# Performance work log

Hardware: AMD Instinct MI355X
Metric: run time of the kernel (lower is better)

Reference implementation:

```python
import jax, jax.numpy as jnp
import numpy as np

B, T, D, L, H = 16, 2048, 512, 6, 1024  # batch, seq, embed_dim, num_layers, mlp hidden (2*D)
K = D // 2  # freq bands; k = min(D//2, T//2) = 256 here
VOCAB = 256


def _ln(x, g, b, eps=1e-5):
    m = x.mean(-1, keepdims=True)
    v = ((x - m) ** 2).mean(-1, keepdims=True)
    return (x - m) / jnp.sqrt(v + eps) * g + b


def setup_inputs() -> dict:
    key = jax.random.key(0)
    ks = jax.random.split(key, 12)
    s = 0.02
    return {
        "byte_ids": jax.random.randint(ks[0], (B, T), 0, 256),
        # ByteSpectralEmbedding params
        "freq_bands": jnp.ones((K,), jnp.float32),
        "fp_w1": jax.random.normal(ks[1], (D, 2 * D), jnp.float32) * s,
        "fp_b1": jnp.zeros((2 * D,), jnp.float32),
        "fp_ln_g": jnp.ones((2 * D,), jnp.float32),
        "fp_ln_b": jnp.zeros((2 * D,), jnp.float32),
        "fp_w2": jax.random.normal(ks[2], (2 * D, D), jnp.float32) * s,
        "fp_b2": jnp.zeros((D,), jnp.float32),
        # SpectralMLPBlock params, stacked over L layers (FNet-style spectral mixing + MLP)
        "blk_ln1_g": jnp.ones((L, D), jnp.float32),
        "blk_ln1_b": jnp.zeros((L, D), jnp.float32),
        "blk_ln2_g": jnp.ones((L, D), jnp.float32),
        "blk_ln2_b": jnp.zeros((L, D), jnp.float32),
        "blk_w1": jax.random.normal(ks[3], (L, D, H), jnp.float32) * s,
        "blk_b1": jnp.zeros((L, H), jnp.float32),
        "blk_w2": jax.random.normal(ks[4], (L, H, D), jnp.float32) * s,
        "blk_b2": jnp.zeros((L, D), jnp.float32),
        # final norm + output head
        "norm_g": jnp.ones((D,), jnp.float32),
        "norm_b": jnp.zeros((D,), jnp.float32),
        "out_w": jax.random.normal(ks[5], (D, VOCAB), jnp.float32) * s,
        "out_b": jnp.zeros((VOCAB,), jnp.float32),
    }


def reference(byte_ids, freq_bands, fp_w1, fp_b1, fp_ln_g, fp_ln_b, fp_w2, fp_b2,
              blk_ln1_g, blk_ln1_b, blk_ln2_g, blk_ln2_b, blk_w1, blk_b1, blk_w2, blk_b2,
              norm_g, norm_b, out_w, out_b):
    Bc, Tc = byte_ids.shape
    k = min(D // 2, Tc // 2)
    signal = byte_ids.astype(jnp.float32) / 127.5 - 1.0          # [B,T]
    X = jnp.fft.fft(signal, axis=1)[:, :k]                        # [B,k] single FFT
    # shift theorem: FFT(roll(signal, -p))[f] = X[f] * exp(+2pi i f p / T)
    mag = jnp.abs(X) * freq_bands[:k]                             # [B,k], position-independent
    base_phase = jnp.angle(X)                                     # [B,k]
    pos = jnp.arange(Tc, dtype=jnp.float32)
    f = jnp.arange(k, dtype=jnp.float32)
    phase = base_phase[:, None, :] + (2.0 * jnp.pi / Tc) * pos[None, :, None] * f[None, None, :]  # [B,T,k]
    mag_bt = jnp.broadcast_to(mag[:, None, :], (Bc, Tc, k))
    feats = jnp.concatenate([mag_bt, jnp.sin(phase), jnp.cos(phase)], axis=-1)
    feats = feats[..., :D] if feats.shape[-1] >= D else jnp.pad(feats, ((0, 0), (0, 0), (0, D - feats.shape[-1])))
    # freq_proj: Linear -> LayerNorm -> GELU -> Linear
    h = feats @ fp_w1 + fp_b1
    h = jax.nn.gelu(_ln(h, fp_ln_g, fp_ln_b), approximate=False)
    x = h @ fp_w2 + fp_b2                                         # [B,T,D]
    # SpectralMLPBlock stack: residual FFT mixing + residual MLP
    for i in range(L):
        y = _ln(x, blk_ln1_g[i], blk_ln1_b[i])
        x = x + jnp.fft.fft(jnp.fft.fft(y, axis=-1), axis=1).real
        y = _ln(x, blk_ln2_g[i], blk_ln2_b[i])
        x = x + jax.nn.gelu(y @ blk_w1[i] + blk_b1[i], approximate=False) @ blk_w2[i] + blk_b2[i]
    x = _ln(x, norm_g, norm_b)
    return x @ out_w + out_b                                      # [B,T,256]
```

## Files before the change

kernel.cpp:

```cpp
#include <hip/hip_runtime.h>
#include <cmath>

typedef unsigned short u16;
typedef unsigned int u32;

constexpr int NB = 16;
constexpr int NT = 2048;
constexpr int ND = 512;
constexpr int NL = 6;
constexpr int NH = 1024;
constexpr int NK = 256;
constexpr int NM = NB * NT;

constexpr float PI2 = 6.283185307179586f;

typedef short bf16x8 __attribute__((ext_vector_type(8)));
typedef float f32x4 __attribute__((ext_vector_type(4)));

__device__ __forceinline__ float gelu_exact(float v) {
    return 0.5f * v * (1.0f + erff(v * 0.70710678118654752f));
}

__device__ __forceinline__ u16 f2bf(float f) {
    union { float f; u32 u; } v; v.f = f;
    u32 r = v.u + 0x7FFFu + ((v.u >> 16) & 1u);
    return (u16)(r >> 16);
}

__device__ __forceinline__ float bf2f(u16 h) {
    union { u32 u; float f; } v; v.u = ((u32)h) << 16;
    return v.f;
}

__device__ __forceinline__ float block_sum256(float val, float* lds4) {
#pragma unroll
    for (int o = 32; o > 0; o >>= 1) val += __shfl_down(val, o);
    int lane = threadIdx.x & 63, wid = threadIdx.x >> 6;
    if (lane == 0) lds4[wid] = val;
    __syncthreads();
    float t = lds4[0] + lds4[1] + lds4[2] + lds4[3];
    __syncthreads();
    return t;
}

__device__ __forceinline__ void swz_block(int& row0, int& col0) {
    int nwg = gridDim.x * gridDim.y;
    int wg = blockIdx.x + blockIdx.y * gridDim.x;
    int L = wg;
    if ((nwg & 7) == 0) {
        int q = nwg >> 3;
        L = (wg & 7) * q + (wg >> 3);
    }
    int ncol = gridDim.y;
    row0 = (L / ncol) * 128;
    col0 = (L % ncol) * 128;
}

__global__ void twiddle_kernel(float2* __restrict__ tw) {
    int idx = blockIdx.x * 256 + threadIdx.x;
    if (idx < 2047) {
        u32 v = idx + 1;
        u32 h = 1u << (31 - __clz(v));
        u32 k = v - h;
        float a = -(float)M_PI * (float)k / (float)h;
        tw[idx] = make_float2(cosf(a), sinf(a));
    }
}

__global__ void dft_kernel(const int* __restrict__ bytes, const float* __restrict__ fb,
                           float* __restrict__ mag, float* __restrict__ cph,
                           float* __restrict__ sph) {
    __shared__ float lr[4], li[4];
    int b = blockIdx.x, f = blockIdx.y;
    float re = 0.f, im = 0.f;
    for (int t = threadIdx.x; t < NT; t += 256) {
        float s = (float)bytes[b * NT + t] * (1.0f / 127.5f) - 1.0f;
        int idx = (t * f) & (NT - 1);
        float a = (float)idx * (PI2 / NT);
        float sn, cs;
        sincosf(a, &sn, &cs);
        re += s * cs;
        im -= s * sn;
    }
#pragma unroll
    for (int o = 32; o > 0; o >>= 1) {
        re += __shfl_down(re, o);
        im += __shfl_down(im, o);
    }
    int lane = threadIdx.x & 63, wid = threadIdx.x >> 6;
    if (lane == 0) { lr[wid] = re; li[wid] = im; }
    __syncthreads();
    if (threadIdx.x == 0) {
        float R = lr[0] + lr[1] + lr[2] + lr[3];
        float I = li[0] + li[1] + li[2] + li[3];
        float m = sqrtf(R * R + I * I);
        mag[b * NK + f] = m * fb[f];
        float inv = (m > 0.f) ? 1.0f / m : 0.f;
        cph[b * NK + f] = (m > 0.f) ? R * inv : 1.0f;
        sph[b * NK + f] = I * inv;
    }
}

__global__ void feats_split_kernel(const float* __restrict__ mag,
                                   const float* __restrict__ cph,
                                   const float* __restrict__ sph,
                                   u16* __restrict__ hi, u16* __restrict__ lo) {
    int idx = blockIdx.x * 256 + threadIdx.x;
    int d = idx & (ND - 1);
    int m = idx >> 9;
    int b = m >> 11, t = m & (NT - 1);
    float v;
    if (d < NK) {
        v = mag[b * NK + d];
    } else {
        int f = d - NK;
        int a = (t * f) & (NT - 1);
        float sn, cs;
        sincosf((float)a * (PI2 / NT), &sn, &cs);
        v = sph[b * NK + f] * cs + cph[b * NK + f] * sn;
    }
    u16 h = f2bf(v);
    hi[idx] = h;
    lo[idx] = f2bf(v - bf2f(h));
}

template <int NV, int GELU, int OBF>
__global__ void ln_kernel(const float* __restrict__ in, const float* __restrict__ g,
                          const float* __restrict__ bta, void* __restrict__ outv) {
    __shared__ float lds4[4];
    constexpr int NE = NV / 256;
    size_t row = blockIdx.x;
    const float* p = in + row * NV;
    float v[NE];
    float sum = 0.f;
#pragma unroll
    for (int i = 0; i < NE; ++i) {
        v[i] = p[threadIdx.x + 256 * i];
        sum += v[i];
    }
    sum = block_sum256(sum, lds4);
    float mean = sum * (1.0f / NV);
    float sq = 0.f;
#pragma unroll
    for (int i = 0; i < NE; ++i) {
        float d = v[i] - mean;
        sq += d * d;
    }
    sq = block_sum256(sq, lds4);
    float inv = rsqrtf(sq * (1.0f / NV) + 1e-5f);
#pragma unroll
    for (int i = 0; i < NE; ++i) {
        int c = threadIdx.x + 256 * i;
        float r = (v[i] - mean) * inv * g[c] + bta[c];
        if (GELU) r = gelu_exact(r);
        if (OBF == 2) {
            u16* o = (u16*)outv + row * (2 * NV);
            u16 hb = f2bf(r);
            o[c] = hb;
            o[NV + c] = f2bf(r - bf2f(hb));
        } else if (OBF == 1) {
            ((u16*)outv)[row * NV + c] = f2bf(r);
        } else {
            ((float*)outv)[row * NV + c] = r;
        }
    }
}

__global__ void ln_fftd_kernel(const float* __restrict__ x, const float* __restrict__ g,
                               const float* __restrict__ bta, float* __restrict__ P,
                               const float2* __restrict__ twid) {
    __shared__ float sr[2][512], si[2][512];
    __shared__ float red[2][2];
    int sub = threadIdx.x >> 7;
    int tid = threadIdx.x & 127;
    int rlocal = blockIdx.x * 2 + sub;
    const float* p = x + (size_t)rlocal * ND;
    float v[4];
    float s = 0.f;
#pragma unroll
    for (int j = 0; j < 4; ++j) { v[j] = p[tid + 128 * j]; s += v[j]; }
#pragma unroll
    for (int o = 32; o > 0; o >>= 1) s += __shfl_down(s, o);
    int wv = (threadIdx.x >> 6) & 1;
    if ((threadIdx.x & 63) == 0) red[sub][wv] = s;
    __syncthreads();
    float mean = (red[sub][0] + red[sub][1]) * (1.0f / ND);
    float q = 0.f;
#pragma unroll
    for (int j = 0; j < 4; ++j) { float d = v[j] - mean; q += d * d; }
#pragma unroll
    for (int o = 32; o > 0; o >>= 1) q += __shfl_down(q, o);
    __syncthreads();
    if ((threadIdx.x & 63) == 0) red[sub][wv] = q;
    __syncthreads();
    float inv = rsqrtf((red[sub][0] + red[sub][1]) * (1.0f / ND) + 1e-5f);
#pragma unroll
    for (int j = 0; j < 4; ++j) {
        int i = tid + 128 * j;
        int r = __brev((unsigned)i) >> 23;
        sr[sub][r] = (v[j] - mean) * inv * g[i] + bta[i];
        si[sub][r] = 0.f;
    }
    __syncthreads();
    for (int len = 2; len <= 512; len <<= 1) {
        int half = len >> 1;
        for (int qq = tid; qq < 256; qq += 128) {
            int k = qq & (half - 1);
            int j = ((qq - k) << 1) + k;
            float2 tw = twid[(half - 1) + k];
            float cs = tw.x, sn = tw.y;
            float ur = sr[sub][j], ui = si[sub][j];
            float vr = sr[sub][j + half], vi = si[sub][j + half];
            float tr = vr * cs - vi * sn;
            float ti = vr * sn + vi * cs;
            sr[sub][j] = ur + tr;
            si[sub][j] = ui + ti;
            sr[sub][j + half] = ur - tr;
            si[sub][j + half] = ui - ti;
        }
        __syncthreads();
    }
    float* out = P + (size_t)rlocal * ND;
    for (int i = tid; i < 512; i += 128)
        out[i] = (i <= 256) ? sr[sub][i] : si[sub][i - 256];
}

__global__ void transpose_bt_kernel(const float* __restrict__ P, float* __restrict__ PT) {
    __shared__ float tile[32][33];
    int b = blockIdx.z, t0 = blockIdx.x * 32, d0 = blockIdx.y * 32;
    int j = threadIdx.x & 31, i0 = threadIdx.x >> 5;
    for (int i = i0; i < 32; i += 8)
        tile[i][j] = P[((size_t)(b * NT + t0 + i)) * ND + d0 + j];
    __syncthreads();
    for (int i = i0; i < 32; i += 8)
        PT[((size_t)(b * ND + d0 + i)) * NT + t0 + j] = tile[j][i];
}

__global__ void fft_t2048_kernel(const float* __restrict__ PT, float* __restrict__ Mt,
                                 const float2* __restrict__ twid) {
    __shared__ float sr[2048], si[2048];
    int b = blockIdx.x;
    int d = blockIdx.y;
    const float* zr = PT + ((size_t)(b * ND + d)) * NT;
    const float* zi = PT + ((size_t)(b * ND + 256 + d)) * NT;
    bool has_im = (d != 0) && (d != 256);
    for (int t = threadIdx.x; t < 2048; t += 256) {
        int r = __brev((unsigned)t) >> 21;
        sr[r] = zr[t];
        si[r] = has_im ? zi[t] : 0.f;
    }
    __syncthreads();
    for (int len = 2; len <= 2048; len <<= 1) {
        int half = len >> 1;
        for (int q = threadIdx.x; q < 1024; q += 256) {
            int k = q & (half - 1);
            int j = ((q - k) << 1) + k;
            float2 tw = twid[(half - 1) + k];
            float cs = tw.x, sn = tw.y;
            float ur = sr[j], ui = si[j];
            float vr = sr[j + half], vi = si[j + half];
            float tr = vr * cs - vi * sn;
            float ti = vr * sn + vi * cs;
            sr[j] = ur + tr;
            si[j] = ui + ti;
            sr[j + half] = ur - tr;
            si[j + half] = ui - ti;
        }
        __syncthreads();
    }
    float* m0 = Mt + ((size_t)(b * ND + d)) * NT;
    for (int t = threadIdx.x; t < 2048; t += 256) m0[t] = sr[t];
    if (has_im) {
        float* m1 = Mt + ((size_t)(b * ND + (512 - d))) * NT;
        for (int t = threadIdx.x; t < 2048; t += 256) m1[t] = sr[(2048 - t) & 2047];
    }
}

__global__ void add_transpose_kernel(const float* __restrict__ Mt, float* __restrict__ x) {
    __shared__ float tile[32][33];
    int b = blockIdx.z, t0 = blockIdx.x * 32, d0 = blockIdx.y * 32;
    int j = threadIdx.x & 31, i0 = threadIdx.x >> 5;
    for (int i = i0; i < 32; i += 8)
        tile[i][j] = Mt[((size_t)(b * ND + d0 + i)) * NT + t0 + j];
    __syncthreads();
    for (int i = i0; i < 32; i += 8) {
        size_t xi = ((size_t)(b * NT + t0 + i)) * ND + d0 + j;
        x[xi] += tile[j][i];
    }
}

__global__ void wconv_kernel(const float* __restrict__ W, u16* __restrict__ Wt,
                             int K, int N) {
    __shared__ float tile[32][33];
    size_t moff = (size_t)blockIdx.z * K * N;
    int n0 = blockIdx.x * 32, k0 = blockIdx.y * 32;
    int j = threadIdx.x & 31, i0 = threadIdx.x >> 5;
    for (int i = i0; i < 32; i += 8)
        tile[i][j] = W[moff + (size_t)(k0 + i) * N + n0 + j];
    __syncthreads();
    for (int i = i0; i < 32; i += 8)
        Wt[moff + (size_t)(n0 + i) * K + k0 + j] = f2bf(tile[j][i]);
}

template <int GELU, int ACC, int OBF, int ADDB>
__global__ __launch_bounds__(256) void mfma_gemm(
    const u16* __restrict__ A, int lda, const u16* __restrict__ Wt,
    const float* __restrict__ bias, void* __restrict__ Cv, int Kd, int Nd) {
    __shared__ __align__(16) u16 Al[2][4096];
    __shared__ __align__(16) u16 Bl[2][4096];
    int tid = threadIdx.x;
    int row0, col0;
    swz_block(row0, col0);
    int lane = tid & 63, w = tid >> 6;
    int wr = w >> 1, wc = w & 1;
    int kg = lane >> 4, ln16 = lane & 15;

    f32x4 acc[4][4] = {};

    auto stage = [&](int buf, int t) {
        int k0 = t << 5;
#pragma unroll
        for (int i = 0; i < 2; ++i) {
            int s = i * 256 + tid;
            int skg = s >> 7, r = s & 127;
            const u16* ga = A + (size_t)(row0 + r) * lda + k0 + skg * 8;
            __builtin_amdgcn_global_load_lds(
                (const __attribute__((address_space(1))) void*)ga,
                (__attribute__((address_space(3))) void*)&Al[buf][s * 8], 16, 0, 0);
            const u16* gb = Wt + (size_t)(col0 + r) * Kd + k0 + skg * 8;
            __builtin_amdgcn_global_load_lds(
                (const __attribute__((address_space(1))) void*)gb,
                (__attribute__((address_space(3))) void*)&Bl[buf][s * 8], 16, 0, 0);
        }
    };
    auto compute = [&](int buf) {
        bf16x8 af[4], bfr[4];
#pragma unroll
        for (int mi = 0; mi < 4; ++mi)
            af[mi] = *(const bf16x8*)&Al[buf][(kg * 128 + wr * 64 + mi * 16 + ln16) * 8];
#pragma unroll
        for (int ni = 0; ni < 4; ++ni)
            bfr[ni] = *(const bf16x8*)&Bl[buf][(kg * 128 + wc * 64 + ni * 16 + ln16) * 8];
#pragma unroll
        for (int mi = 0; mi < 4; ++mi)
#pragma unroll
            for (int ni = 0; ni < 4; ++ni)
                acc[mi][ni] = __builtin_amdgcn_mfma_f32_16x16x32_bf16(
                    af[mi], bfr[ni], acc[mi][ni], 0, 0, 0);
    };

    int nt = Kd >> 5;
    stage(0, 0);
    __syncthreads();
    int cur = 0;
    for (int t = 1; t < nt; ++t) {
        stage(cur ^ 1, t);
        compute(cur);
        __syncthreads();
        cur ^= 1;
    }
    compute(cur);

#pragma unroll
    for (int mi = 0; mi < 4; ++mi) {
#pragma unroll
        for (int ni = 0; ni < 4; ++ni) {
            int col = col0 + wc * 64 + ni * 16 + ln16;
            float bv = ADDB ? bias[col] : 0.f;
#pragma unroll
            for (int j = 0; j < 4; ++j) {
                int row = row0 + wr * 64 + mi * 16 + kg * 4 + j;
                float v = acc[mi][ni][j] + bv;
                if (GELU) v = gelu_exact(v);
                size_t o = (size_t)row * Nd + col;
                if (OBF) {
                    ((u16*)Cv)[o] = f2bf(v);
                } else {
                    float* C = (float*)Cv;
                    if (ACC) v += C[o];
                    C[o] = v;
                }
            }
        }
    }
}

__global__ __launch_bounds__(256) void mfma_gemm2(
    const u16* __restrict__ Ahi, const u16* __restrict__ Alo, int lda,
    const u16* __restrict__ Wt, const float* __restrict__ bias,
    float* __restrict__ C, int Kd, int Nd) {
    __shared__ __align__(16) u16 Ah[3][4096];
    __shared__ __align__(16) u16 Al2[3][4096];
    __shared__ __align__(16) u16 Bl[3][4096];
    int tid = threadIdx.x;
    int row0, col0;
    swz_block(row0, col0);
    int lane = tid & 63, w = tid >> 6;
    int wr = w >> 1, wc = w & 1;
    int kg = lane >> 4, ln16 = lane & 15;

    f32x4 acc[4][4] = {};

    auto stage = [&](int buf, int t) {
        int k0 = t << 5;
#pragma unroll
        for (int i = 0; i < 2; ++i) {
            int s = i * 256 + tid;
            int skg = s >> 7, r = s & 127;
            size_t aoff = (size_t)(row0 + r) * lda + k0 + skg * 8;
            __builtin_amdgcn_global_load_lds(
                (const __attribute__((address_space(1))) void*)(Ahi + aoff),
                (__attribute__((address_space(3))) void*)&Ah[buf][s * 8], 16, 0, 0);
            __builtin_amdgcn_global_load_lds(
                (const __attribute__((address_space(1))) void*)(Alo + aoff),
                (__attribute__((address_space(3))) void*)&Al2[buf][s * 8], 16, 0, 0);
            const u16* gb = Wt + (size_t)(col0 + r) * Kd + k0 + skg * 8;
            __builtin_amdgcn_global_load_lds(
                (const __attribute__((address_space(1))) void*)gb,
                (__attribute__((address_space(3))) void*)&Bl[buf][s * 8], 16, 0, 0);
        }
    };
    auto compute = [&](int buf) {
        bf16x8 ah[4], al[4], bfr[4];
#pragma unroll
        for (int mi = 0; mi < 4; ++mi) {
            int sl = (kg * 128 + wr * 64 + mi * 16 + ln16) * 8;
            ah[mi] = *(const bf16x8*)&Ah[buf][sl];
            al[mi] = *(const bf16x8*)&Al2[buf][sl];
        }
#pragma unroll
        for (int ni = 0; ni < 4; ++ni)
            bfr[ni] = *(const bf16x8*)&Bl[buf][(kg * 128 + wc * 64 + ni * 16 + ln16) * 8];
#pragma unroll
        for (int mi = 0; mi < 4; ++mi)
#pragma unroll
            for (int ni = 0; ni < 4; ++ni) {
                acc[mi][ni] = __builtin_amdgcn_mfma_f32_16x16x32_bf16(
                    ah[mi], bfr[ni], acc[mi][ni], 0, 0, 0);
                acc[mi][ni] = __builtin_amdgcn_mfma_f32_16x16x32_bf16(
                    al[mi], bfr[ni], acc[mi][ni], 0, 0, 0);
            }
    };

    int nt = Kd >> 5;
    stage(0, 0);
    stage(1, 1);
    for (int t = 0; t < nt; ++t) {
        if (t + 1 < nt) asm volatile("s_waitcnt vmcnt(6)" ::: "memory");
        else            asm volatile("s_waitcnt vmcnt(0)" ::: "memory");
        __builtin_amdgcn_sched_barrier(0);
        __builtin_amdgcn_s_barrier();
        __builtin_amdgcn_sched_barrier(0);
        if (t + 2 < nt) stage((t + 2) % 3, t + 2);
        compute(t % 3);
    }

#pragma unroll
    for (int mi = 0; mi < 4; ++mi) {
#pragma unroll
        for (int ni = 0; ni < 4; ++ni) {
            int col = col0 + wc * 64 + ni * 16 + ln16;
            float bv = bias[col];
#pragma unroll
            for (int j = 0; j < 4; ++j) {
                int row = row0 + wr * 64 + mi * 16 + kg * 4 + j;
                C[(size_t)row * Nd + col] = acc[mi][ni][j] + bv;
            }
        }
    }
}

extern "C" void kernel_launch(void* const* d_in, const int* in_sizes, int n_in,
                              void* d_out, int out_size, void* d_ws, size_t ws_size,
                              hipStream_t stream) {
    const int* byte_ids     = (const int*)d_in[0];
    const float* freq_bands = (const float*)d_in[1];
    const float* fp_w1   = (const float*)d_in[2];
    const float* fp_b1   = (const float*)d_in[3];
    const float* fp_ln_g = (const float*)d_in[4];
    const float* fp_ln_b = (const float*)d_in[5];
    const float* fp_w2   = (const float*)d_in[6];
    const float* fp_b2   = (const float*)d_in[7];
    const float* blk_ln1_g = (const float*)d_in[8];
    const float* blk_ln1_b = (const float*)d_in[9];
    const float* blk_ln2_g = (const float*)d_in[10];
    const float* blk_ln2_b = (const float*)d_in[11];
    const float* blk_w1  = (const float*)d_in[12];
    const float* blk_b1  = (const float*)d_in[13];
    const float* blk_w2  = (const float*)d_in[14];
    const float* blk_b2  = (const float*)d_in[15];
    const float* norm_g  = (const float*)d_in[16];
    const float* norm_b  = (const float*)d_in[17];
    const float* out_w   = (const float*)d_in[18];
    const float* out_b   = (const float*)d_in[19];
    float* out = (float*)d_out;
    char* base = (char*)d_ws;
    char* obase = (char*)d_out;
    const size_t MB = 1048576;

    u16* fhi     = (u16*)base;
    u16* flo     = (u16*)(base + 32 * MB);
    float* xA    = (float*)base;
    float* hfp   = (float*)(base + 64 * MB);
    u16* h2      = (u16*)hfp;
    float* Zbuf  = (float*)(base + 64 * MB);
    float* PTbuf = (float*)(base + 128 * MB);
    float* Mtbuf = Zbuf;
    u16* hmlp    = (u16*)(base + 64 * MB);
    u16* ybf     = (u16*)(base + 128 * MB);
    u16* outwt   = (u16*)(base + 64 * MB);
    u16* fpw1t   = (u16*)obase;
    u16* fpw2t   = (u16*)(obase + 1 * MB);
    float* mag   = (float*)(obase + 2 * MB);
    float* cph   = mag + NB * NK;
    float* sph   = cph + NB * NK;
    float2* twid = (float2*)(obase + 4 * MB);
    u16* blkw1t  = (u16*)(obase + 6 * MB);
    u16* blkw2t  = (u16*)(obase + 12 * MB);

    twiddle_kernel<<<8, 256, 0, stream>>>(twid);

    dft_kernel<<<dim3(NB, NK), 256, 0, stream>>>(byte_ids, freq_bands, mag, cph, sph);
    feats_split_kernel<<<(NM * ND) / 256, 256, 0, stream>>>(mag, cph, sph, fhi, flo);
    wconv_kernel<<<dim3(NH / 32, ND / 32, 1), 256, 0, stream>>>(fp_w1, fpw1t, ND, NH);
    wconv_kernel<<<dim3(ND / 32, NH / 32, 1), 256, 0, stream>>>(fp_w2, fpw2t, NH, ND);
    wconv_kernel<<<dim3(NH / 32, ND / 32, NL), 256, 0, stream>>>(blk_w1, blkw1t, ND, NH);
    wconv_kernel<<<dim3(ND / 32, NH / 32, NL), 256, 0, stream>>>(blk_w2, blkw2t, NH, ND);

    mfma_gemm2<<<dim3(NM / 128, NH / 128), 256, 0, stream>>>(
        fhi, flo, ND, fpw1t, fp_b1, hfp, ND, NH);
    ln_kernel<NH, 1, 2><<<NM, 256, 0, stream>>>(hfp, fp_ln_g, fp_ln_b, h2);
    mfma_gemm2<<<dim3(NM / 128, ND / 128), 256, 0, stream>>>(
        h2, h2 + NH, 2 * NH, fpw2t, fp_b2, xA, NH, ND);

    for (int l = 0; l < NL; ++l) {
        ln_fftd_kernel<<<NM / 2, 256, 0, stream>>>(
            xA, blk_ln1_g + l * ND, blk_ln1_b + l * ND, Zbuf, twid);
        transpose_bt_kernel<<<dim3(NT / 32, ND / 32, NB), 256, 0, stream>>>(Zbuf, PTbuf);
        fft_t2048_kernel<<<dim3(NB, 257), 256, 0, stream>>>(PTbuf, Mtbuf, twid);
        add_transpose_kernel<<<dim3(NT / 32, ND / 32, NB), 256, 0, stream>>>(Mtbuf, xA);
        ln_kernel<ND, 0, 1><<<NM, 256, 0, stream>>>(
            xA, blk_ln2_g + l * ND, blk_ln2_b + l * ND, ybf);
        mfma_gemm<1, 0, 1, 1><<<dim3(NM / 128, NH / 128), 256, 0, stream>>>(
            ybf, ND, blkw1t + (size_t)l * ND * NH, blk_b1 + l * NH, hmlp, ND, NH);
        mfma_gemm<0, 1, 0, 1><<<dim3(NM / 128, ND / 128), 256, 0, stream>>>(
            hmlp, NH, blkw2t + (size_t)l * ND * NH, blk_b2 + l * ND, xA, NH, ND);
    }

    ln_kernel<ND, 0, 1><<<NM, 256, 0, stream>>>(xA, norm_g, norm_b, ybf);
    wconv_kernel<<<dim3(256 / 32, ND / 32, 1), 256, 0, stream>>>(out_w, outwt, ND, 256);
    mfma_gemm<0, 0, 0, 1><<<dim3(NM / 128, 256 / 128), 256, 0, stream>>>(
        ybf, ND, outwt, out_b, out, ND, 256);
}
```

Measured before the change: 2.919 ms.

## Fuse residual add-transpose with LayerNorm and make row FFT one wave per row

The transpose-back residual add is merged with the following LayerNorm into a single kernel. Each block loads a 16-timestep by 512-channel tile of the FFT output into LDS, adds it to x, and writes both the updated x and the bf16 normalized activations, which saves one full pass over x per layer. Separately, the per-row LN+FFT kernel now gives each 512-point row to a single 64-lane wavefront, four rows per block, so block-wide syncs are replaced by wave shuffles. The uncoalesced strided loads from Mt in the fused kernel, and the reliance on wavefront lockstep for LDS ordering in the FFT, are the main risks.

Measured after the change: 2.807 ms. -3.8%, faster.

```diff
diff --git a/kernel.cpp b/kernel.cpp
--- a/kernel.cpp
+++ b/kernel.cpp
@@ -169,60 +169,56 @@
 __global__ void ln_fftd_kernel(const float* __restrict__ x, const float* __restrict__ g,
                                const float* __restrict__ bta, float* __restrict__ P,
                                const float2* __restrict__ twid) {
-    __shared__ float sr[2][512], si[2][512];
-    __shared__ float red[2][2];
-    int sub = threadIdx.x >> 7;
-    int tid = threadIdx.x & 127;
-    int rlocal = blockIdx.x * 2 + sub;
+    __shared__ float sr[4][512], si[4][512];
+    int wv = threadIdx.x >> 6, lane = threadIdx.x & 63;
+    int rlocal = blockIdx.x * 4 + wv;
     const float* p = x + (size_t)rlocal * ND;
-    float v[4];
+    float v[8];
     float s = 0.f;
 #pragma unroll
-    for (int j = 0; j < 4; ++j) { v[j] = p[tid + 128 * j]; s += v[j]; }
+    for (int j = 0; j < 8; ++j) { v[j] = p[lane + 64 * j]; s += v[j]; }
 #pragma unroll
     for (int o = 32; o > 0; o >>= 1) s += __shfl_down(s, o);
-    int wv = (threadIdx.x >> 6) & 1;
-    if ((threadIdx.x & 63) == 0) red[sub][wv] = s;
-    __syncthreads();
-    float mean = (red[sub][0] + red[sub][1]) * (1.0f / ND);
+    s = __shfl(s, 0);
+    float mean = s * (1.0f / ND);
     float q = 0.f;
 #pragma unroll
-    for (int j = 0; j < 4; ++j) { float d = v[j] - mean; q += d * d; }
+    for (int j = 0; j < 8; ++j) { float d = v[j] - mean; q += d * d; }
 #pragma unroll
     for (int o = 32; o > 0; o >>= 1) q += __shfl_down(q, o);
-    __syncthreads();
-    if ((threadIdx.x & 63) == 0) red[sub][wv] = q;
-    __syncthreads();
-    float inv = rsqrtf((red[sub][0] + red[sub][1]) * (1.0f / ND) + 1e-5f);
-#pragma unroll
-    for (int j = 0; j < 4; ++j) {
-        int i = tid + 128 * j;
+    q = __shfl(q, 0);
+    float inv = rsqrtf(q * (1.0f / ND) + 1e-5f);
+#pragma unroll
+    for (int j = 0; j < 8; ++j) {
+        int i = lane + 64 * j;
         int r = __brev((unsigned)i) >> 23;
-        sr[sub][r] = (v[j] - mean) * inv * g[i] + bta[i];
-        si[sub][r] = 0.f;
-    }
-    __syncthreads();
+        sr[wv][r] = (v[j] - mean) * inv * g[i] + bta[i];
+        si[wv][r] = 0.f;
+    }
     for (int len = 2; len <= 512; len <<= 1) {
         int half = len >> 1;
-        for (int qq = tid; qq < 256; qq += 128) {
+#pragma unroll
+        for (int qq = lane; qq < 256; qq += 64) {
             int k = qq & (half - 1);
             int j = ((qq - k) << 1) + k;
             float2 tw = twid[(half - 1) + k];
             float cs = tw.x, sn = tw.y;
-            float ur = sr[sub][j], ui = si[sub][j];
-            float vr = sr[sub][j + half], vi = si[sub][j + half];
+            float ur = sr[wv][j], ui = si[wv][j];
+            float vr = sr[wv][j + half], vi = si[wv][j + half];
             float tr = vr * cs - vi * sn;
             float ti = vr * sn + vi * cs;
-            sr[sub][j] = ur + tr;
-            si[sub][j] = ui + ti;
-            sr[sub][j + half] = ur - tr;
-            si[sub][j + half] = ui - ti;
-        }
-        __syncthreads();
+            sr[wv][j] = ur + tr;
+            si[wv][j] = ui + ti;
+            sr[wv][j + half] = ur - tr;
+            si[wv][j + half] = ui - ti;
+        }
     }
     float* out = P + (size_t)rlocal * ND;
-    for (int i = tid; i < 512; i += 128)
-        out[i] = (i <= 256) ? sr[sub][i] : si[sub][i - 256];
+#pragma unroll
+    for (int j = 0; j < 8; ++j) {
+        int i = lane + 64 * j;
+        out[i] = (i <= 256) ? sr[wv][i] : si[wv][i - 256];
+    }
 }
 
 __global__ void transpose_bt_kernel(const float* __restrict__ P, float* __restrict__ PT) {
@@ -276,16 +272,47 @@
     }
 }
 
-__global__ void add_transpose_kernel(const float* __restrict__ Mt, float* __restrict__ x) {
-    __shared__ float tile[32][33];
-    int b = blockIdx.z, t0 = blockIdx.x * 32, d0 = blockIdx.y * 32;
-    int j = threadIdx.x & 31, i0 = threadIdx.x >> 5;
-    for (int i = i0; i < 32; i += 8)
-        tile[i][j] = Mt[((size_t)(b * ND + d0 + i)) * NT + t0 + j];
-    __syncthreads();
-    for (int i = i0; i < 32; i += 8) {
-        size_t xi = ((size_t)(b * NT + t0 + i)) * ND + d0 + j;
-        x[xi] += tile[j][i];
+__global__ void addt_ln_kernel(const float* __restrict__ Mt, float* __restrict__ x,
+                               const float* __restrict__ g, const float* __restrict__ bta,
+                               u16* __restrict__ yb) {
+    __shared__ float tile[512 * 17];
+    int b = blockIdx.y, t0 = blockIdx.x * 16;
+    int tid = threadIdx.x;
+    for (int lin = tid; lin < 512 * 16; lin += 256) {
+        int tloc = lin & 15, d = lin >> 4;
+        tile[d * 17 + tloc] = Mt[((size_t)(b * ND + d)) * NT + t0 + tloc];
+    }
+    __syncthreads();
+    int lane = tid & 63, wv = tid >> 6;
+#pragma unroll
+    for (int rr = 0; rr < 4; ++rr) {
+        int tloc = wv * 4 + rr;
+        size_t row = (size_t)(b * NT + t0 + tloc);
+        float v[8];
+        float s = 0.f;
+#pragma unroll
+        for (int e = 0; e < 8; ++e) {
+            int d = lane + 64 * e;
+            v[e] = x[row * ND + d] + tile[d * 17 + tloc];
+            s += v[e];
+        }
+#pragma unroll
+        for (int o = 32; o > 0; o >>= 1) s += __shfl_down(s, o);
+        s = __shfl(s, 0);
+        float mean = s * (1.0f / ND);
+        float q = 0.f;
+#pragma unroll
+        for (int e = 0; e < 8; ++e) { float d2 = v[e] - mean; q += d2 * d2; }
+#pragma unroll
+        for (int o = 32; o > 0; o >>= 1) q += __shfl_down(q, o);
+        q = __shfl(q, 0);
+        float inv = rsqrtf(q * (1.0f / ND) + 1e-5f);
+#pragma unroll
+        for (int e = 0; e < 8; ++e) {
+            int d = lane + 64 * e;
+            x[row * ND + d] = v[e];
+            yb[row * ND + d] = f2bf((v[e] - mean) * inv * g[d] + bta[d]);
+        }
     }
 }
 
@@ -534,13 +561,12 @@
         h2, h2 + NH, 2 * NH, fpw2t, fp_b2, xA, NH, ND);
 
     for (int l = 0; l < NL; ++l) {
-        ln_fftd_kernel<<<NM / 2, 256, 0, stream>>>(
+        ln_fftd_kernel<<<NM / 4, 256, 0, stream>>>(
             xA, blk_ln1_g + l * ND, blk_ln1_b + l * ND, Zbuf, twid);
         transpose_bt_kernel<<<dim3(NT / 32, ND / 32, NB), 256, 0, stream>>>(Zbuf, PTbuf);
         fft_t2048_kernel<<<dim3(NB, 257), 256, 0, stream>>>(PTbuf, Mtbuf, twid);
-        add_transpose_kernel<<<dim3(NT / 32, ND / 32, NB), 256, 0, stream>>>(Mtbuf, xA);
-        ln_kernel<ND, 0, 1><<<NM, 256, 0, stream>>>(
-            xA, blk_ln2_g + l * ND, blk_ln2_b + l * ND, ybf);
+        addt_ln_kernel<<<dim3(NT / 16, NB), 256, 0, stream>>>(
+            Mtbuf, xA, blk_ln2_g + l * ND, blk_ln2_b + l * ND, ybf);
         mfma_gemm<1, 0, 1, 1><<<dim3(NM / 128, NH / 128), 256, 0, stream>>>(
             ybf, ND, blkw1t + (size_t)l * ND * NH, blk_b1 + l * NH, hmlp, ND, NH);
         mfma_gemm<0, 1, 0, 1><<<dim3(NM / 128, ND / 128), 256, 0, stream>>>(
```
